# Kernel optimization log

Hardware: AMD Instinct MI355X
Metric: run time of the kernel (lower is better)

## Reference

```python
import jax, jax.numpy as jnp
import numpy as np

B, A, BOARD, D = 64, 32, 64, 5
TAU_FAC, TAU_INH = 50.0, 20.0
LR_FAC, LR_INH = 0.0002, 0.0001
COLL_WINDOW = 10.0
SAFE_THRESH = 0.7
ALIGN_THRESH = 0.6


def setup_inputs() -> dict:
    key = jax.random.key(0)
    ks = jax.random.split(key, 7)
    positions = jax.random.uniform(ks[0], (B, A, 2), jnp.float32, 0.0, BOARD)
    goals = jax.random.uniform(ks[1], (B, A, 2), jnp.float32, 0.0, BOARD)
    spike_outputs = jax.random.uniform(ks[2], (B, A, D), jnp.float32)
    fac_traces = jax.random.uniform(ks[3], (B, A, BOARD, BOARD, D), jnp.float32)
    inh_traces = jax.random.uniform(ks[4], (B, A, BOARD, BOARD, D), jnp.float32)
    collision_history = jax.random.uniform(ks[5], (B, A, BOARD, BOARD), jnp.float32)
    collisions = jax.random.bernoulli(ks[6], 0.2, (B, A))
    return {"positions": positions, "goals": goals, "spike_outputs": spike_outputs,
            "fac_traces": fac_traces, "inh_traces": inh_traces,
            "collision_history": collision_history, "collisions": collisions}


def reference(positions, goals, spike_outputs, fac_traces, inh_traces,
              collision_history, collisions):
    # action deltas for the 5 movement directions
    deltas = jnp.array([[0, 0], [1, 0], [0, 1], [-1, 0], [0, -1]], jnp.float32)

    # 1) exponential STDP trace decay (bulk elementwise over 5D tensors)
    fac = fac_traces * jnp.exp(-1.0 / TAU_FAC)
    inh = inh_traces * jnp.exp(-1.0 / TAU_INH)

    # 2) collision history: decay + scatter-add at clamped integer positions
    pos_i = positions.astype(jnp.int32)                        # torch .long() truncation (positions >= 0)
    x = jnp.clip(pos_i[..., 0], 0, BOARD - 1)                  # [B, A]
    y = jnp.clip(pos_i[..., 1], 0, BOARD - 1)
    bi = jnp.arange(collision_history.shape[0])[:, None]
    ai = jnp.arange(collision_history.shape[1])[None, :]
    ch = collision_history * (1.0 - 1.0 / COLL_WINDOW)
    ch = ch.at[bi, ai, y, x].add(collisions.astype(jnp.float32) / COLL_WINDOW)

    # 3) region safety: gather collision rate at each agent's cell
    safety = 1.0 - jnp.clip(ch[bi, ai, y, x], 0.0, 1.0)        # [B, A]

    # 4) goal alignment for all directions at once
    gv = goals - positions                                     # [B, A, 2]
    gvn = gv / (jnp.linalg.norm(gv, axis=-1, keepdims=True) + 1e-8)
    align = (jnp.einsum('bav,dv->bad', gvn, deltas) + 1.0) / 2.0  # [B, A, D]

    # 5) facilitation / inhibition conditions and position-indexed scatter updates
    spike_cond = spike_outputs > 0.5
    safe = (safety > SAFE_THRESH)[..., None]
    fac_cond = spike_cond & safe & (align > ALIGN_THRESH)
    inh_cond = spike_cond & (~safe | (align <= 1.0 - ALIGN_THRESH))
    fac = fac.at[bi, ai, y, x].add(LR_FAC * fac_cond.astype(jnp.float32))
    inh = inh.at[bi, ai, y, x].add(LR_INH * inh_cond.astype(jnp.float32))

    return fac, inh, ch, safety
```

## Files before the change

### kernel.cpp

```cpp
#include <hip/hip_runtime.h>

static constexpr int B_ = 64, A_ = 32, BOARD_ = 64, D_ = 5;
static constexpr long long FACN = (long long)B_ * A_ * BOARD_ * BOARD_ * D_;
static constexpr long long CHN  = (long long)B_ * A_ * BOARD_ * BOARD_;
static constexpr int NAG = B_ * A_;

static constexpr float FAC_DECAY = 0.9801986733067553f;
static constexpr float INH_DECAY = 0.9512294245007140f;

typedef float f32x4 __attribute__((ext_vector_type(4)));

__global__ __launch_bounds__(256) void bulk_kernel(
    const f32x4* __restrict__ fac_in, const f32x4* __restrict__ inh_in,
    const f32x4* __restrict__ ch_in, f32x4* __restrict__ out)
{
    const int FACV = (int)(FACN / 4);
    const int C = 11264;
    const int t = threadIdx.x;
    const int base = blockIdx.x * C;

    for (int off = 0; off < C; off += 1024) {
        const int G = base + off;
        const f32x4* __restrict__ s;
        float c;
        if (G < FACV)            { s = fac_in + G;            c = FAC_DECAY; }
        else if (G < 2 * FACV)   { s = inh_in + (G - FACV);   c = INH_DECAY; }
        else                     { s = ch_in + (G - 2 * FACV); c = 0.9f; }
        f32x4* __restrict__ d = out + G;

        f32x4 a = __builtin_nontemporal_load(&s[t]);
        f32x4 b = __builtin_nontemporal_load(&s[t + 256]);
        f32x4 e = __builtin_nontemporal_load(&s[t + 512]);
        f32x4 f = __builtin_nontemporal_load(&s[t + 768]);
        a *= c; b *= c; e *= c; f *= c;
        __builtin_nontemporal_store(a, &d[t]);
        __builtin_nontemporal_store(b, &d[t + 256]);
        __builtin_nontemporal_store(e, &d[t + 512]);
        __builtin_nontemporal_store(f, &d[t + 768]);
    }
}

__global__ __launch_bounds__(64) void agent_kernel(
    const float* __restrict__ pos, const float* __restrict__ goal,
    const float* __restrict__ spike,
    const float* __restrict__ fac_in, const float* __restrict__ inh_in,
    const float* __restrict__ ch_in,
    const void* __restrict__ coll,
    float* __restrict__ out)
{
    __shared__ int s_w4, s_h2;
    if (threadIdx.x == 0) { s_w4 = 1; s_h2 = 1; }
    __syncthreads();
    {
        const unsigned int* cw = (const unsigned int*)coll;
        for (int k = threadIdx.x; k < 512; k += 64) {
            unsigned int w = cw[k];
            if (!(w == 0u || w == 1u || w == 0x3F800000u)) s_w4 = 0;
            unsigned int lo = w & 0xFFFFu, hi = w >> 16;
            if (!((lo == 0u || lo == 1u || lo == 0x3F80u || lo == 0x3C00u) &&
                  (hi == 0u || hi == 1u || hi == 0x3F80u || hi == 0x3C00u)))
                s_h2 = 0;
        }
    }
    __syncthreads();
    const int f = s_w4 ? 4 : (s_h2 ? 2 : 1);

    int idx = blockIdx.x * blockDim.x + threadIdx.x;
    if (idx >= NAG) return;

    float px = pos[idx * 2 + 0];
    float py = pos[idx * 2 + 1];
    int x = min(BOARD_ - 1, max(0, (int)px));
    int y = min(BOARD_ - 1, max(0, (int)py));
    long long cell = ((long long)idx * BOARD_ + y) * BOARD_ + x;

    bool c;
    if (f == 4)      c = ((const unsigned int*)coll)[idx] != 0u;
    else if (f == 2) c = ((const unsigned short*)coll)[idx] != 0u;
    else             c = ((const unsigned char*)coll)[idx] != 0u;

    float chv = ch_in[cell] * 0.9f + (c ? 0.1f : 0.0f);
    const long long CHOFF  = 2 * FACN;
    const long long SAFOFF = CHOFF + CHN;
    out[CHOFF + cell] = chv;
    float safety = 1.0f - fminf(fmaxf(chv, 0.0f), 1.0f);
    out[SAFOFF + idx] = safety;
    bool safe = safety > 0.7f;

    float gx = goal[idx * 2 + 0] - px;
    float gy = goal[idx * 2 + 1] - py;
    float n = sqrtf(gx * gx + gy * gy) + 1e-8f;
    float gnx = gx / n, gny = gy / n;
    float align[5];
    align[0] = 0.5f;
    align[1] = (gnx + 1.0f) * 0.5f;
    align[2] = (gny + 1.0f) * 0.5f;
    align[3] = (1.0f - gnx) * 0.5f;
    align[4] = (1.0f - gny) * 0.5f;

    long long cd = cell * D_;
#pragma unroll
    for (int d = 0; d < D_; ++d) {
        bool sp = spike[idx * D_ + d] > 0.5f;
        bool fc = sp && safe && (align[d] > 0.6f);
        bool ic = sp && (!safe || (align[d] <= 0.4f));
        float fv = fac_in[cd + d] * FAC_DECAY + (fc ? 0.0002f : 0.0f);
        float iv = inh_in[cd + d] * INH_DECAY + (ic ? 0.0001f : 0.0f);
        out[cd + d] = fv;
        out[FACN + cd + d] = iv;
    }
}

extern "C" void kernel_launch(void* const* d_in, const int* in_sizes, int n_in,
                              void* d_out, int out_size, void* d_ws, size_t ws_size,
                              hipStream_t stream) {
    const float* pos   = (const float*)d_in[0];
    const float* goal  = (const float*)d_in[1];
    const float* spike = (const float*)d_in[2];
    const float* fac   = (const float*)d_in[3];
    const float* inh   = (const float*)d_in[4];
    const float* ch    = (const float*)d_in[5];
    const void*  coll  = d_in[6];
    float* out = (float*)d_out;

    hipLaunchKernelGGL(bulk_kernel, dim3(2048), dim3(256), 0, stream,
                       (const f32x4*)fac, (const f32x4*)inh, (const f32x4*)ch, (f32x4*)out);
    hipLaunchKernelGGL(agent_kernel, dim3(32), dim3(64), 0, stream,
                       pos, goal, spike, fac, inh, ch, coll, out);
}
```

Baseline: 146.3 us.

## Software-pipeline bulk loads and spread agent updates across threads per direction

The bulk decay kernel now issues the loads for the next 1024-vector group before storing the current one, so memory reads overlap with writes inside each thread. The agent kernel now uses eight threads per agent instead of one: five handle one direction each and a sixth writes collision history and safety. It launches 256 blocks instead of 32. Both changes aim to hide memory latency in a bandwidth-bound pass and in a small latency-bound tail kernel, at the cost of more registers in the bulk loop.

```diff
diff --git a/kernel.cpp b/kernel.cpp
--- a/kernel.cpp
+++ b/kernel.cpp
@@ -19,24 +19,32 @@
     const int t = threadIdx.x;
     const int base = blockIdx.x * C;
 
-    for (int off = 0; off < C; off += 1024) {
-        const int G = base + off;
+    auto ldgrp = [&](int G, f32x4 v[4], float& c) {
         const f32x4* __restrict__ s;
-        float c;
-        if (G < FACV)            { s = fac_in + G;            c = FAC_DECAY; }
-        else if (G < 2 * FACV)   { s = inh_in + (G - FACV);   c = INH_DECAY; }
-        else                     { s = ch_in + (G - 2 * FACV); c = 0.9f; }
-        f32x4* __restrict__ d = out + G;
+        if (G < FACV)          { s = fac_in + G;             c = FAC_DECAY; }
+        else if (G < 2 * FACV) { s = inh_in + (G - FACV);    c = INH_DECAY; }
+        else                   { s = ch_in + (G - 2 * FACV); c = 0.9f; }
+        v[0] = __builtin_nontemporal_load(&s[t]);
+        v[1] = __builtin_nontemporal_load(&s[t + 256]);
+        v[2] = __builtin_nontemporal_load(&s[t + 512]);
+        v[3] = __builtin_nontemporal_load(&s[t + 768]);
+    };
 
-        f32x4 a = __builtin_nontemporal_load(&s[t]);
-        f32x4 b = __builtin_nontemporal_load(&s[t + 256]);
-        f32x4 e = __builtin_nontemporal_load(&s[t + 512]);
-        f32x4 f = __builtin_nontemporal_load(&s[t + 768]);
-        a *= c; b *= c; e *= c; f *= c;
-        __builtin_nontemporal_store(a, &d[t]);
-        __builtin_nontemporal_store(b, &d[t + 256]);
-        __builtin_nontemporal_store(e, &d[t + 512]);
-        __builtin_nontemporal_store(f, &d[t + 768]);
+    f32x4 v[4]; float c;
+    ldgrp(base, v, c);
+    int off = 0;
+    while (true) {
+        f32x4 w[4]; float c2;
+        const int noff = off + 1024;
+        if (noff < C) ldgrp(base + noff, w, c2);
+        f32x4* __restrict__ d = out + base + off;
+        __builtin_nontemporal_store(v[0] * c, &d[t]);
+        __builtin_nontemporal_store(v[1] * c, &d[t + 256]);
+        __builtin_nontemporal_store(v[2] * c, &d[t + 512]);
+        __builtin_nontemporal_store(v[3] * c, &d[t + 768]);
+        if (noff >= C) break;
+        v[0] = w[0]; v[1] = w[1]; v[2] = w[2]; v[3] = w[3]; c = c2;
+        off = noff;
     }
 }
 
@@ -65,8 +73,10 @@
     __syncthreads();
     const int f = s_w4 ? 4 : (s_h2 ? 2 : 1);
 
-    int idx = blockIdx.x * blockDim.x + threadIdx.x;
-    if (idx >= NAG) return;
+    const int tid = blockIdx.x * 64 + threadIdx.x;
+    const int idx = tid >> 3;
+    const int d   = tid & 7;
+    if (idx >= NAG || d >= 6) return;
 
     float px = pos[idx * 2 + 0];
     float py = pos[idx * 2 + 1];
@@ -80,35 +90,34 @@
     else             c = ((const unsigned char*)coll)[idx] != 0u;
 
     float chv = ch_in[cell] * 0.9f + (c ? 0.1f : 0.0f);
-    const long long CHOFF  = 2 * FACN;
-    const long long SAFOFF = CHOFF + CHN;
-    out[CHOFF + cell] = chv;
     float safety = 1.0f - fminf(fmaxf(chv, 0.0f), 1.0f);
-    out[SAFOFF + idx] = safety;
+
+    if (d == 5) {
+        const long long CHOFF  = 2 * FACN;
+        const long long SAFOFF = CHOFF + CHN;
+        out[CHOFF + cell] = chv;
+        out[SAFOFF + idx] = safety;
+        return;
+    }
+
     bool safe = safety > 0.7f;
 
     float gx = goal[idx * 2 + 0] - px;
     float gy = goal[idx * 2 + 1] - py;
     float n = sqrtf(gx * gx + gy * gy) + 1e-8f;
     float gnx = gx / n, gny = gy / n;
-    float align[5];
-    align[0] = 0.5f;
-    align[1] = (gnx + 1.0f) * 0.5f;
-    align[2] = (gny + 1.0f) * 0.5f;
-    align[3] = (1.0f - gnx) * 0.5f;
-    align[4] = (1.0f - gny) * 0.5f;
+    float al = (d == 0) ? 0.5f
+             : (d == 1) ? (gnx + 1.0f) * 0.5f
+             : (d == 2) ? (gny + 1.0f) * 0.5f
+             : (d == 3) ? (1.0f - gnx) * 0.5f
+                        : (1.0f - gny) * 0.5f;
 
-    long long cd = cell * D_;
-#pragma unroll
-    for (int d = 0; d < D_; ++d) {
-        bool sp = spike[idx * D_ + d] > 0.5f;
-        bool fc = sp && safe && (align[d] > 0.6f);
-        bool ic = sp && (!safe || (align[d] <= 0.4f));
-        float fv = fac_in[cd + d] * FAC_DECAY + (fc ? 0.0002f : 0.0f);
-        float iv = inh_in[cd + d] * INH_DECAY + (ic ? 0.0001f : 0.0f);
-        out[cd + d] = fv;
-        out[FACN + cd + d] = iv;
-    }
+    long long cd = cell * D_ + d;
+    bool sp = spike[idx * D_ + d] > 0.5f;
+    bool fc = sp && safe && (al > 0.6f);
+    bool ic = sp && (!safe || (al <= 0.4f));
+    out[cd]        = fac_in[cd] * FAC_DECAY + (fc ? 0.0002f : 0.0f);
+    out[FACN + cd] = inh_in[cd] * INH_DECAY + (ic ? 0.0001f : 0.0f);
 }
 
 extern "C" void kernel_launch(void* const* d_in, const int* in_sizes, int n_in,
@@ -125,6 +134,6 @@
 
     hipLaunchKernelGGL(bulk_kernel, dim3(2048), dim3(256), 0, stream,
                        (const f32x4*)fac, (const f32x4*)inh, (const f32x4*)ch, (f32x4*)out);
-    hipLaunchKernelGGL(agent_kernel, dim3(32), dim3(64), 0, stream,
+    hipLaunchKernelGGL(agent_kernel, dim3(256), dim3(64), 0, stream,
                        pos, goal, spike, fac, inh, ch, coll, out);
 }
```

Result: no change. 144.6 us (-1.2%).
